# Kernel optimization log

Hardware: AMD Instinct MI355X
Metric: run time of the kernel (lower is better)

The kernel has to match this reference:

```python
import jax, jax.numpy as jnp
import numpy as np

NUM_EMBEDDINGS = 1024
EMBEDDING_DIM = 64
COMMITMENT_COST = 0.25


def setup_inputs() -> dict:
    key = jax.random.key(0)
    k1, k2 = jax.random.split(key)
    z = jax.random.normal(k1, (16, EMBEDDING_DIM, 64, 64), dtype=jnp.float32)
    # nn.Embedding init: uniform(-1/K, 1/K)
    emb = jax.random.uniform(
        k2, (NUM_EMBEDDINGS, EMBEDDING_DIM), dtype=jnp.float32,
        minval=-1.0 / NUM_EMBEDDINGS, maxval=1.0 / NUM_EMBEDDINGS)
    return {"z": z, "emb": emb}


def reference(z, emb):
    # b c h w -> b h w c
    zc = jnp.transpose(z, (0, 2, 3, 1))
    B, H, W, D = zc.shape
    zf = zc.reshape(-1, D)  # [N, D]
    K = emb.shape[0]

    # L2 distances: ||z||^2 + ||e||^2 - 2 z e^T   -> [N, K]
    distances = (jnp.sum(zf * zf, axis=1, keepdims=True)
                 + jnp.sum(emb * emb, axis=1)
                 - 2.0 * jnp.matmul(zf, emb.T))
    encoding_indices = jnp.argmin(distances, axis=1)  # [N]

    # one_hot @ emb  ==  gather
    quantized = emb[encoding_indices].reshape(zc.shape)  # [B,H,W,D]

    reconstruction_errors = jnp.sum((quantized - zc) ** 2, axis=-1).reshape(-1)
    avg_error = jnp.mean(reconstruction_errors)

    e_latent_loss = jnp.mean((jax.lax.stop_gradient(quantized) - zc) ** 2)
    q_latent_loss = jnp.mean((quantized - jax.lax.stop_gradient(zc)) ** 2)
    loss = q_latent_loss + COMMITMENT_COST * e_latent_loss

    # straight-through estimator
    quantized_st = zc + jax.lax.stop_gradient(quantized - zc)
    out = jnp.transpose(quantized_st, (0, 3, 1, 2))  # b h w c -> b c h w

    # perplexity: avg one-hot usage (histogram instead of dense one-hot)
    N = zf.shape[0]
    counts = jnp.zeros((K,), dtype=jnp.float32).at[encoding_indices].add(1.0)
    avg_probs = counts / N
    perplexity = jnp.exp(-jnp.sum(avg_probs * jnp.log(avg_probs + 1e-10)))

    return out, loss, perplexity, avg_error
```

## Files before the change

### kernel.cpp

```cpp
#include <hip/hip_runtime.h>
#include <stdint.h>

#define HW   4096
#define NEMB 1024

typedef float        f32x4  __attribute__((ext_vector_type(4)));
typedef short        h16x8  __attribute__((ext_vector_type(8)));
typedef unsigned int u32x4  __attribute__((ext_vector_type(4)));

#define CVTPKH(D, LO, HI) asm("v_cvt_pkrtz_f16_f32 %0, %1, %2" : "=v"(D) : "v"(LO), "v"(HI))

__device__ __forceinline__ void gload_lds16(const float* g, float* l) {
    __builtin_amdgcn_global_load_lds(
        (const __attribute__((address_space(1))) void*)(uintptr_t)g,
        (__attribute__((address_space(3))) void*)(uintptr_t)l, 16, 0, 0);
}

__global__ __launch_bounds__(128) void vq_init(const float* __restrict__ emb,
                                               unsigned int* __restrict__ counts,
                                               float* __restrict__ errsum,
                                               float* __restrict__ ens1,
                                               unsigned int* __restrict__ embh) {
    const int k = blockIdx.x * 128 + threadIdx.x;
    counts[k] = 0u;
    if (k == 0) *errsum = 0.0f;
    const float* e = emb + k * 64;
    unsigned int* dst = embh + k * 32;
    float a[8] = {0,0,0,0,0,0,0,0};
    #pragma unroll
    for (int c = 0; c < 8; ++c) {
        f32x4 v0 = *(const f32x4*)(e + c * 8);
        f32x4 v1 = *(const f32x4*)(e + c * 8 + 4);
        a[0] += v0.x * v0.x; a[1] += v0.y * v0.y;
        a[2] += v0.z * v0.z; a[3] += v0.w * v0.w;
        a[4] += v1.x * v1.x; a[5] += v1.y * v1.y;
        a[6] += v1.z * v1.z; a[7] += v1.w * v1.w;
        u32x4 w;
        CVTPKH(w.x, v0.x, v0.y); CVTPKH(w.y, v0.z, v0.w);
        CVTPKH(w.z, v1.x, v1.y); CVTPKH(w.w, v1.z, v1.w);
        *(u32x4*)&dst[c * 4] = w;
    }
    ens1[k] = 1.0f + (((a[0]+a[1]) + (a[2]+a[3])) + ((a[4]+a[5]) + (a[6]+a[7])));
}

__global__ __launch_bounds__(512, 4)
void vq_main(const float* __restrict__ z, const float* __restrict__ emb,
             const float* __restrict__ ens1, const unsigned int* __restrict__ embh,
             float* __restrict__ out, unsigned int* __restrict__ counts,
             float* __restrict__ errsum)
{
    __shared__ __attribute__((aligned(16))) float z_lds[64 * 128];
    __shared__ __attribute__((aligned(16))) unsigned int zh[128 * 32];
    __shared__ __attribute__((aligned(16))) float ens_lds[NEMB];
    __shared__ unsigned int kd[8][128];
    __shared__ int   idx_sh[128];
    __shared__ float errp[512];

    const int t   = threadIdx.x;
    const int n0  = blockIdx.x * 128;
    const int bb  = n0 >> 12;
    const int hw0 = n0 & 4095;
    const float* zb = z + bb * (64 * HW) + hw0;

    #pragma unroll
    for (int it = 0; it < 4; ++it) {
        const int p = it * 512 + t;
        gload_lds16(zb + (p >> 5) * HW + (p & 31) * 4, z_lds + p * 4);
    }
    if (t < 256) gload_lds16(ens1 + t * 4, ens_lds + t * 4);
    __syncthreads();

    {
        const int x = t & 127;
        #pragma unroll
        for (int ss = 0; ss < 2; ++ss) {
            const int s = (x + (t >> 7) * 2 + ss) & 7;
            const int c = s ^ (x & 7);
            u32x4 w;
            CVTPKH(w.x, z_lds[(8*c + 0) * 128 + x], z_lds[(8*c + 1) * 128 + x]);
            CVTPKH(w.y, z_lds[(8*c + 2) * 128 + x], z_lds[(8*c + 3) * 128 + x]);
            CVTPKH(w.z, z_lds[(8*c + 4) * 128 + x], z_lds[(8*c + 5) * 128 + x]);
            CVTPKH(w.w, z_lds[(8*c + 6) * 128 + x], z_lds[(8*c + 7) * 128 + x]);
            *(u32x4*)&zh[x * 32 + s * 4] = w;
        }
    }

    const int l   = t & 63;
    const int wv  = t >> 6;
    const int col = l & 15;
    const int bg  = l >> 4;

    u32x4 bw0[8], bw1[8];
    {
        const unsigned int* ebase = embh + (wv * 128 + col) * 32 + bg * 4;
        #pragma unroll
        for (int g = 0; g < 8; ++g) {
            bw0[g] = *(const u32x4*)(ebase + g * 16 * 32);
            bw1[g] = *(const u32x4*)(ebase + g * 16 * 32 + 16);
        }
    }
    float en[8];
    #pragma unroll
    for (int g = 0; g < 8; ++g) en[g] = ens_lds[wv * 128 + g * 16 + col];

    __syncthreads();

    const unsigned int lkc = (unsigned int)col;
    #pragma unroll 1
    for (int st = 0; st < 8; ++st) {
        const int xs = st * 16 + col;
        const int sA = bg ^ (col & 7);
        u32x4 wa = *(const u32x4*)&zh[xs * 32 + sA * 4];
        u32x4 wb = *(const u32x4*)&zh[xs * 32 + (sA ^ 4) * 4];
        h16x8 a0 = __builtin_bit_cast(h16x8, wa);
        h16x8 a1 = __builtin_bit_cast(h16x8, wb);

        unsigned int k0 = ~0u, k1 = ~0u, k2 = ~0u, k3 = ~0u;
        #pragma unroll
        for (int g = 0; g < 8; ++g) {
            f32x4 cc = {0.0f, 0.0f, 0.0f, 0.0f};
            cc = __builtin_amdgcn_mfma_f32_16x16x32_f16(a0, __builtin_bit_cast(h16x8, bw0[g]), cc, 0, 0, 0);
            cc = __builtin_amdgcn_mfma_f32_16x16x32_f16(a1, __builtin_bit_cast(h16x8, bw1[g]), cc, 0, 0, 0);
            const unsigned int lk = (unsigned int)(g << 4) | lkc;
            float s0 = fmaf(-2.0f, cc[0], en[g]);
            float s1 = fmaf(-2.0f, cc[1], en[g]);
            float s2 = fmaf(-2.0f, cc[2], en[g]);
            float s3 = fmaf(-2.0f, cc[3], en[g]);
            unsigned int q0 = (__builtin_bit_cast(unsigned int, s0) & ~127u) | lk;
            unsigned int q1 = (__builtin_bit_cast(unsigned int, s1) & ~127u) | lk;
            unsigned int q2 = (__builtin_bit_cast(unsigned int, s2) & ~127u) | lk;
            unsigned int q3 = (__builtin_bit_cast(unsigned int, s3) & ~127u) | lk;
            k0 = k0 < q0 ? k0 : q0;  k1 = k1 < q1 ? k1 : q1;
            k2 = k2 < q2 ? k2 : q2;  k3 = k3 < q3 ? k3 : q3;
        }
        #pragma unroll
        for (int mk = 1; mk <= 8; mk <<= 1) {
            unsigned int o0 = (unsigned int)__shfl_xor((int)k0, mk, 64);
            unsigned int o1 = (unsigned int)__shfl_xor((int)k1, mk, 64);
            unsigned int o2 = (unsigned int)__shfl_xor((int)k2, mk, 64);
            unsigned int o3 = (unsigned int)__shfl_xor((int)k3, mk, 64);
            k0 = k0 < o0 ? k0 : o0;  k1 = k1 < o1 ? k1 : o1;
            k2 = k2 < o2 ? k2 : o2;  k3 = k3 < o3 ? k3 : o3;
        }
        if (col == 0) {
            u32x4 kv = {k0, k1, k2, k3};
            *(u32x4*)&kd[wv][st * 16 + bg * 4] = kv;
        }
    }
    __syncthreads();

    if (t < 128) {
        unsigned int kw = kd[0][t];
        unsigned int bv = kw & ~127u;
        int bk = (int)(kw & 127u);
        #pragma unroll
        for (int w = 1; w < 8; ++w) {
            kw = kd[w][t];
            unsigned int vw = kw & ~127u;
            int kk = w * 128 + (int)(kw & 127u);
            if (vw < bv || (vw == bv && kk < bk)) { bv = vw; bk = kk; }
        }
        idx_sh[t] = bk;
        atomicAdd(&counts[bk], 1u);
    }
    __syncthreads();

    {
        const int x  = t & 127;
        const int cg = t >> 7;
        const int idx = idx_sh[x];
        const float* er = emb + idx * 64;
        float* ob = out + bb * (64 * HW) + hw0 + x;
        float part = 0.0f;
        #pragma unroll
        for (int cq = 0; cq < 4; ++cq) {
            const int c = cg * 16 + cq * 4;
            f32x4 e4 = *(const f32x4*)&er[c];
            float z0 = z_lds[(c+0) * 128 + x];
            float z1 = z_lds[(c+1) * 128 + x];
            float z2 = z_lds[(c+2) * 128 + x];
            float z3 = z_lds[(c+3) * 128 + x];
            ob[(c+0) * HW] = z0 + (e4.x - z0);
            ob[(c+1) * HW] = z1 + (e4.y - z1);
            ob[(c+2) * HW] = z2 + (e4.z - z2);
            ob[(c+3) * HW] = z3 + (e4.w - z3);
            float d0 = z0 - e4.x, d1 = z1 - e4.y, d2 = z2 - e4.z, d3 = z3 - e4.w;
            part = fmaf(d0, d0, part); part = fmaf(d1, d1, part);
            part = fmaf(d2, d2, part); part = fmaf(d3, d3, part);
        }
        errp[t] = part;
    }
    __syncthreads();
    if (t < 128) {
        float s = (errp[t] + errp[t + 128]) + (errp[t + 256] + errp[t + 384]);
        #pragma unroll
        for (int off = 32; off >= 1; off >>= 1) s += __shfl_down(s, off, 64);
        if ((t & 63) == 0) atomicAdd(errsum, s);
    }
}

__global__ __launch_bounds__(256) void vq_fin(const unsigned int* __restrict__ counts,
                                              const float* __restrict__ errsum,
                                              float* __restrict__ scal)
{
    __shared__ float part[4];
    const int t = threadIdx.x;
    float s = 0.0f;
    for (int k = t; k < NEMB; k += 256) {
        float p = (float)counts[k] * (1.0f / 65536.0f);
        s += p * logf(p + 1e-10f);
    }
    #pragma unroll
    for (int off = 32; off >= 1; off >>= 1) s += __shfl_down(s, off, 64);
    if ((t & 63) == 0) part[t >> 6] = s;
    __syncthreads();
    if (t == 0) {
        float tot = (part[0] + part[1]) + (part[2] + part[3]);
        float es  = *errsum;
        scal[0] = 1.25f * (es * (1.0f / 4194304.0f));
        scal[1] = expf(-tot);
        scal[2] = es * (1.0f / 65536.0f);
    }
}

extern "C" void kernel_launch(void* const* d_in, const int* in_sizes, int n_in,
                              void* d_out, int out_size, void* d_ws, size_t ws_size,
                              hipStream_t stream) {
    const float* z   = (const float*)d_in[0];
    const float* emb = (const float*)d_in[1];
    float* out = (float*)d_out;
    unsigned int* counts = (unsigned int*)d_ws;
    float* errsum = (float*)((char*)d_ws + 4096);
    float* ens1   = (float*)((char*)d_ws + 8192);
    unsigned int* embh = (unsigned int*)((char*)d_ws + 16384);

    vq_init<<<8, 128, 0, stream>>>(emb, counts, errsum, ens1, embh);
    vq_main<<<512, 512, 0, stream>>>(z, emb, ens1, embh, out, counts, errsum);
    vq_fin<<<1, 256, 0, stream>>>(counts, errsum, out + 4194304);
}
```

Measured before the change: 44.13 us.

## Fold finalize kernel into main via last-block atomic counter and restructure loads

Removes the separate vq_fin launch: each block atomically increments a flag after adding its error partial, and the last block computes perplexity and losses. Also splits vq_init across two threads per embedding row, issues the codebook register loads before the first barrier so they overlap the z LDS fill, reads norms straight from global memory instead of LDS, and splits the two MFMAs into independent accumulators to shorten the dependency chain. The error reduction is now per-wave shuffles plus a small shared array. Risks include the threadfence/atomic ordering correctness and serial tail work in the last block.

After: 56.25 us. +27.5%, slower.

```diff
diff --git a/kernel.cpp b/kernel.cpp
--- a/kernel.cpp
+++ b/kernel.cpp
@@ -20,41 +20,43 @@
                                                unsigned int* __restrict__ counts,
                                                float* __restrict__ errsum,
                                                float* __restrict__ ens1,
-                                               unsigned int* __restrict__ embh) {
-    const int k = blockIdx.x * 128 + threadIdx.x;
-    counts[k] = 0u;
-    if (k == 0) *errsum = 0.0f;
-    const float* e = emb + k * 64;
-    unsigned int* dst = embh + k * 32;
-    float a[8] = {0,0,0,0,0,0,0,0};
+                                               unsigned int* __restrict__ embh,
+                                               unsigned int* __restrict__ flag) {
+    const int gid  = blockIdx.x * 128 + threadIdx.x;
+    const int k    = gid >> 1;
+    const int half = gid & 1;
+    if (half == 0) counts[k] = 0u;
+    if (gid == 0) { *errsum = 0.0f; *flag = 0u; }
+    const float* e = emb + k * 64 + half * 32;
+    unsigned int* dst = embh + k * 32 + half * 16;
+    float nrm = 0.0f;
     #pragma unroll
-    for (int c = 0; c < 8; ++c) {
+    for (int c = 0; c < 4; ++c) {
         f32x4 v0 = *(const f32x4*)(e + c * 8);
         f32x4 v1 = *(const f32x4*)(e + c * 8 + 4);
-        a[0] += v0.x * v0.x; a[1] += v0.y * v0.y;
-        a[2] += v0.z * v0.z; a[3] += v0.w * v0.w;
-        a[4] += v1.x * v1.x; a[5] += v1.y * v1.y;
-        a[6] += v1.z * v1.z; a[7] += v1.w * v1.w;
+        nrm += v0.x*v0.x + v0.y*v0.y + v0.z*v0.z + v0.w*v0.w
+             + v1.x*v1.x + v1.y*v1.y + v1.z*v1.z + v1.w*v1.w;
         u32x4 w;
         CVTPKH(w.x, v0.x, v0.y); CVTPKH(w.y, v0.z, v0.w);
         CVTPKH(w.z, v1.x, v1.y); CVTPKH(w.w, v1.z, v1.w);
         *(u32x4*)&dst[c * 4] = w;
     }
-    ens1[k] = 1.0f + (((a[0]+a[1]) + (a[2]+a[3])) + ((a[4]+a[5]) + (a[6]+a[7])));
+    float o = __shfl_xor(nrm, 1, 64);
+    if (half == 0) ens1[k] = 1.0f + (nrm + o);
 }
 
 __global__ __launch_bounds__(512, 4)
 void vq_main(const float* __restrict__ z, const float* __restrict__ emb,
              const float* __restrict__ ens1, const unsigned int* __restrict__ embh,
              float* __restrict__ out, unsigned int* __restrict__ counts,
-             float* __restrict__ errsum)
+             float* __restrict__ errsum, unsigned int* __restrict__ flag)
 {
     __shared__ __attribute__((aligned(16))) float z_lds[64 * 128];
     __shared__ __attribute__((aligned(16))) unsigned int zh[128 * 32];
-    __shared__ __attribute__((aligned(16))) float ens_lds[NEMB];
     __shared__ unsigned int kd[8][128];
     __shared__ int   idx_sh[128];
-    __shared__ float errp[512];
+    __shared__ float errw[8];
+    __shared__ unsigned int rank_s;
 
     const int t   = threadIdx.x;
     const int n0  = blockIdx.x * 128;
@@ -67,7 +69,25 @@
         const int p = it * 512 + t;
         gload_lds16(zb + (p >> 5) * HW + (p & 31) * 4, z_lds + p * 4);
     }
-    if (t < 256) gload_lds16(ens1 + t * 4, ens_lds + t * 4);
+
+    const int l   = t & 63;
+    const int wv  = t >> 6;
+    const int col = l & 15;
+    const int bg  = l >> 4;
+
+    u32x4 bw0[8], bw1[8];
+    {
+        const unsigned int* ebase = embh + (wv * 128 + col) * 32 + bg * 4;
+        #pragma unroll
+        for (int g = 0; g < 8; ++g) {
+            bw0[g] = *(const u32x4*)(ebase + g * 512);
+            bw1[g] = *(const u32x4*)(ebase + g * 512 + 16);
+        }
+    }
+    float en[8];
+    #pragma unroll
+    for (int g = 0; g < 8; ++g) en[g] = ens1[wv * 128 + g * 16 + col];
+
     __syncthreads();
 
     {
@@ -84,25 +104,6 @@
             *(u32x4*)&zh[x * 32 + s * 4] = w;
         }
     }
-
-    const int l   = t & 63;
-    const int wv  = t >> 6;
-    const int col = l & 15;
-    const int bg  = l >> 4;
-
-    u32x4 bw0[8], bw1[8];
-    {
-        const unsigned int* ebase = embh + (wv * 128 + col) * 32 + bg * 4;
-        #pragma unroll
-        for (int g = 0; g < 8; ++g) {
-            bw0[g] = *(const u32x4*)(ebase + g * 16 * 32);
-            bw1[g] = *(const u32x4*)(ebase + g * 16 * 32 + 16);
-        }
-    }
-    float en[8];
-    #pragma unroll
-    for (int g = 0; g < 8; ++g) en[g] = ens_lds[wv * 128 + g * 16 + col];
-
     __syncthreads();
 
     const unsigned int lkc = (unsigned int)col;
@@ -119,13 +120,14 @@
         #pragma unroll
         for (int g = 0; g < 8; ++g) {
             f32x4 cc = {0.0f, 0.0f, 0.0f, 0.0f};
+            f32x4 cd = {0.0f, 0.0f, 0.0f, 0.0f};
             cc = __builtin_amdgcn_mfma_f32_16x16x32_f16(a0, __builtin_bit_cast(h16x8, bw0[g]), cc, 0, 0, 0);
-            cc = __builtin_amdgcn_mfma_f32_16x16x32_f16(a1, __builtin_bit_cast(h16x8, bw1[g]), cc, 0, 0, 0);
+            cd = __builtin_amdgcn_mfma_f32_16x16x32_f16(a1, __builtin_bit_cast(h16x8, bw1[g]), cd, 0, 0, 0);
             const unsigned int lk = (unsigned int)(g << 4) | lkc;
-            float s0 = fmaf(-2.0f, cc[0], en[g]);
-            float s1 = fmaf(-2.0f, cc[1], en[g]);
-            float s2 = fmaf(-2.0f, cc[2], en[g]);
-            float s3 = fmaf(-2.0f, cc[3], en[g]);
+            float s0 = fmaf(-2.0f, cc[0] + cd[0], en[g]);
+            float s1 = fmaf(-2.0f, cc[1] + cd[1], en[g]);
+            float s2 = fmaf(-2.0f, cc[2] + cd[2], en[g]);
+            float s3 = fmaf(-2.0f, cc[3] + cd[3], en[g]);
             unsigned int q0 = (__builtin_bit_cast(unsigned int, s0) & ~127u) | lk;
             unsigned int q1 = (__builtin_bit_cast(unsigned int, s1) & ~127u) | lk;
             unsigned int q2 = (__builtin_bit_cast(unsigned int, s2) & ~127u) | lk;
@@ -165,13 +167,13 @@
     }
     __syncthreads();
 
+    float part = 0.0f;
     {
         const int x  = t & 127;
         const int cg = t >> 7;
         const int idx = idx_sh[x];
         const float* er = emb + idx * 64;
         float* ob = out + bb * (64 * HW) + hw0 + x;
-        float part = 0.0f;
         #pragma unroll
         for (int cq = 0; cq < 4; ++cq) {
             const int c = cg * 16 + cq * 4;
@@ -188,38 +190,45 @@
             part = fmaf(d0, d0, part); part = fmaf(d1, d1, part);
             part = fmaf(d2, d2, part); part = fmaf(d3, d3, part);
         }
-        errp[t] = part;
-    }
-    __syncthreads();
-    if (t < 128) {
-        float s = (errp[t] + errp[t + 128]) + (errp[t + 256] + errp[t + 384]);
+    }
+    {
+        float s = part;
         #pragma unroll
         for (int off = 32; off >= 1; off >>= 1) s += __shfl_down(s, off, 64);
-        if ((t & 63) == 0) atomicAdd(errsum, s);
-    }
-}
-
-__global__ __launch_bounds__(256) void vq_fin(const unsigned int* __restrict__ counts,
-                                              const float* __restrict__ errsum,
-                                              float* __restrict__ scal)
-{
-    __shared__ float part[4];
-    const int t = threadIdx.x;
-    float s = 0.0f;
-    for (int k = t; k < NEMB; k += 256) {
-        float p = (float)counts[k] * (1.0f / 65536.0f);
-        s += p * logf(p + 1e-10f);
-    }
-    #pragma unroll
-    for (int off = 32; off >= 1; off >>= 1) s += __shfl_down(s, off, 64);
-    if ((t & 63) == 0) part[t >> 6] = s;
+        if (l == 0) errw[wv] = s;
+    }
     __syncthreads();
     if (t == 0) {
-        float tot = (part[0] + part[1]) + (part[2] + part[3]);
-        float es  = *errsum;
-        scal[0] = 1.25f * (es * (1.0f / 4194304.0f));
-        scal[1] = expf(-tot);
-        scal[2] = es * (1.0f / 65536.0f);
+        float es = ((errw[0]+errw[1]) + (errw[2]+errw[3]))
+                 + ((errw[4]+errw[5]) + (errw[6]+errw[7]));
+        atomicAdd(errsum, es);
+        __threadfence();
+        rank_s = atomicAdd(flag, 1u);
+    }
+    __syncthreads();
+
+    if (rank_s == 511u) {
+        __threadfence();
+        float s = 0.0f;
+        #pragma unroll
+        for (int k2 = t; k2 < NEMB; k2 += 512) {
+            unsigned int cv = atomicAdd(&counts[k2], 0u);
+            float p = (float)cv * (1.0f / 65536.0f);
+            s += p * logf(p + 1e-10f);
+        }
+        #pragma unroll
+        for (int off = 32; off >= 1; off >>= 1) s += __shfl_down(s, off, 64);
+        if (l == 0) errw[wv] = s;
+        __syncthreads();
+        if (t == 0) {
+            float tot = ((errw[0]+errw[1]) + (errw[2]+errw[3]))
+                      + ((errw[4]+errw[5]) + (errw[6]+errw[7]));
+            float es = atomicAdd(errsum, 0.0f);
+            float* scal = out + 4194304;
+            scal[0] = 1.25f * (es * (1.0f / 4194304.0f));
+            scal[1] = expf(-tot);
+            scal[2] = es * (1.0f / 65536.0f);
+        }
     }
 }
 
@@ -231,10 +240,10 @@
     float* out = (float*)d_out;
     unsigned int* counts = (unsigned int*)d_ws;
     float* errsum = (float*)((char*)d_ws + 4096);
+    unsigned int* flag = (unsigned int*)((char*)d_ws + 4160);
     float* ens1   = (float*)((char*)d_ws + 8192);
     unsigned int* embh = (unsigned int*)((char*)d_ws + 16384);
 
-    vq_init<<<8, 128, 0, stream>>>(emb, counts, errsum, ens1, embh);
-    vq_main<<<512, 512, 0, stream>>>(z, emb, ens1, embh, out, counts, errsum);
-    vq_fin<<<1, 256, 0, stream>>>(counts, errsum, out + 4194304);
-}
+    vq_init<<<16, 128, 0, stream>>>(emb, counts, errsum, ens1, embh, flag);
+    vq_main<<<512, 512, 0, stream>>>(z, emb, ens1, embh, out, counts, errsum, flag);
+}
```
